# Performance work log

Hardware: AMD Instinct MI355X
Metric: run time of the kernel (lower is better)

Reference implementation:

```python
import jax, jax.numpy as jnp
import numpy as np

MAX_DISP = 4                    # R: max displacement of the correlation window
D = 2 * MAX_DISP + 1            # window side -> D*D = 81 offset channels


def setup_inputs() -> dict:
    key = jax.random.key(0)
    k1, k2 = jax.random.split(key)
    B, C, H, W = 16, 256, 96, 96
    reference_features = jax.random.normal(k1, (B, D * D, H, W), dtype=jnp.float32)
    query_features = jax.random.normal(k2, (B, C, H, W), dtype=jnp.float32)
    return {"reference_features": reference_features, "query_features": query_features}


def reference(reference_features, query_features):
    # reference_features: [B, D*D, H, W] correlation volume (weights per spatial offset)
    # query_features:     [B, C, H, W]  feature map
    # out[b,c,y,x] = sum_{dy,dx in [-R,R]} corr[b, idx(dy,dx), y-dy, x-dx] * feat[b,c,y-dy,x-dx]
    # i.e. the adjoint of local correlation: scatter-accumulate across shifted windows.
    B, D2, H, W = reference_features.shape
    C = query_features.shape[1]
    R = MAX_DISP
    # Padded accumulator so every shifted write stays in-bounds (zero padding semantics).
    acc = jnp.zeros((B, C, H + 2 * R, W + 2 * R), dtype=query_features.dtype)
    for idx in range(D2):  # fixed small offset set (81), not a data-dim loop
        dy = idx // D - R
        dx = idx % D - R
        w = reference_features[:, idx:idx + 1] * query_features  # [B, C, H, W]
        acc = acc.at[:, :, R + dy:R + dy + H, R + dx:R + dx + W].add(w)
    return acc[:, :, R:R + H, R:R + W]
```

## Files before the change

### kernel.cpp

```cpp
#include <hip/hip_runtime.h>


#define RR 4
#define DD 9
#define D2 81
#define Bn 16
#define Cn 256
#define Hn 96
#define Wn 96
#define HWn (Hn*Wn)
#define NTH 512
#define KW  104

typedef __attribute__((ext_vector_type(8))) short bf16x8;
typedef __attribute__((ext_vector_type(4))) float f32x4;

__device__ __forceinline__ ushort f2bf(float f) {
    uint u = __float_as_uint(f);
    return (ushort)((u + 0x7FFFu + ((u >> 16) & 1u)) >> 16);
}

__global__ __launch_bounds__(NTH, 2)
void corrT11_kernel(const float* __restrict__ corr,
                    const float* __restrict__ feat,
                    float* __restrict__ out)
{
    __shared__ ushort A_sh[2][Cn][KW];
    __shared__ ushort M_sh[2][Wn][KW];

    int bid = blockIdx.x;
    int L   = (bid & 7) * 192 + (bid >> 3);
    int y   = L % Hn;
    int b   = L / Hn;

    const int tid  = threadIdx.x;
    const int lane = tid & 63;
    const int wid  = tid >> 6;
    const int mrow = lane & 15;
    const int kgrp = (lane >> 4) << 3;

    {
        uint* p = (uint*)A_sh;
        for (int t = tid; t < (int)(sizeof(A_sh) / 4); t += NTH) p[t] = 0u;
        uint* q = (uint*)M_sh;
        for (int t = tid; t < (int)(sizeof(M_sh) / 4); t += NTH) q[t] = 0u;
    }
    __syncthreads();

    const int klo = max(0, y - (Hn - 1 - RR));
    const int khi = min(DD - 1, y + RR);

    const int ac  = tid >> 1;
    const int seg = tid & 1;
    const float* fbase = feat + (((size_t)b * Cn + ac) * Hn) * Wn + seg * 48;

    {
        const int sy = y + RR - klo;
        const float* src = fbase + (size_t)sy * Wn;
        #pragma unroll
        for (int i = 0; i < 12; ++i) {
            float4 v = *reinterpret_cast<const float4*>(src + i * 4);
            uint lo = (uint)f2bf(v.x) | ((uint)f2bf(v.y) << 16);
            uint hi = (uint)f2bf(v.z) | ((uint)f2bf(v.w) << 16);
            *reinterpret_cast<uint2*>(&A_sh[0][ac][4 + seg * 48 + i * 4]) = make_uint2(lo, hi);
        }
        for (int t = tid; t < DD * Wn; t += NTH) {
            int kdx = t / Wn;
            int x   = t - kdx * Wn;
            int sx  = x + RR - kdx;
            int sxc = min(max(sx, 0), Wn - 1);
            float v = corr[((size_t)b * D2 + klo * DD + kdx) * HWn + sy * Wn + sxc];
            M_sh[0][x][x + 2 * RR - kdx] = f2bf(v);
        }
    }

    f32x4 acc[2][6];
    #pragma unroll
    for (int ct = 0; ct < 2; ++ct)
        #pragma unroll
        for (int xt = 0; xt < 6; ++xt)
            acc[ct][xt] = (f32x4){0.f, 0.f, 0.f, 0.f};

    #pragma unroll 1
    for (int kk = klo; kk <= khi; ++kk) {
        const int pb = (kk - klo) & 1;
        __syncthreads();

        const bool vn = (kk + 1 <= khi);
        float4 fv[12];
        float  mv0 = 0.f, mv1 = 0.f;
        if (vn) {
            const int sy = y + RR - (kk + 1);
            const float* src = fbase + (size_t)sy * Wn;
            #pragma unroll
            for (int i = 0; i < 12; ++i)
                fv[i] = *reinterpret_cast<const float4*>(src + i * 4);
            {
                int t = tid;
                int kdx = t / Wn, x = t - kdx * Wn;
                int sx  = x + RR - kdx;
                int sxc = min(max(sx, 0), Wn - 1);
                mv0 = corr[((size_t)b * D2 + (kk + 1) * DD + kdx) * HWn + sy * Wn + sxc];
            }
            if (tid + NTH < DD * Wn) {
                int t = tid + NTH;
                int kdx = t / Wn, x = t - kdx * Wn;
                int sx  = x + RR - kdx;
                int sxc = min(max(sx, 0), Wn - 1);
                mv1 = corr[((size_t)b * D2 + (kk + 1) * DD + kdx) * HWn + sy * Wn + sxc];
            }
        }

        #pragma unroll
        for (int xt = 0; xt < 6; ++xt) {
            const int kb = (xt == 5) ? 72 : xt * 16;
            bf16x8 bfr = *reinterpret_cast<const bf16x8*>(&M_sh[pb][xt * 16 + mrow][kb + kgrp]);
            #pragma unroll
            for (int ct = 0; ct < 2; ++ct) {
                bf16x8 afr = *reinterpret_cast<const bf16x8*>(&A_sh[pb][wid * 32 + ct * 16 + mrow][kb + kgrp]);
                acc[ct][xt] = __builtin_amdgcn_mfma_f32_16x16x32_bf16(afr, bfr, acc[ct][xt], 0, 0, 0);
            }
        }

        if (vn) {
            #pragma unroll
            for (int i = 0; i < 12; ++i) {
                uint lo = (uint)f2bf(fv[i].x) | ((uint)f2bf(fv[i].y) << 16);
                uint hi = (uint)f2bf(fv[i].z) | ((uint)f2bf(fv[i].w) << 16);
                *reinterpret_cast<uint2*>(&A_sh[pb ^ 1][ac][4 + seg * 48 + i * 4]) = make_uint2(lo, hi);
            }
            {
                int t = tid;
                int kdx = t / Wn, x = t - kdx * Wn;
                M_sh[pb ^ 1][x][x + 2 * RR - kdx] = f2bf(mv0);
            }
            if (tid + NTH < DD * Wn) {
                int t = tid + NTH;
                int kdx = t / Wn, x = t - kdx * Wn;
                M_sh[pb ^ 1][x][x + 2 * RR - kdx] = f2bf(mv1);
            }
        }
    }

    const int csub = (lane >> 4) << 2;
    #pragma unroll
    for (int ct = 0; ct < 2; ++ct) {
        #pragma unroll
        for (int xt = 0; xt < 6; ++xt) {
            #pragma unroll
            for (int r = 0; r < 4; ++r) {
                int c = wid * 32 + ct * 16 + csub + r;
                int x = xt * 16 + mrow;
                out[(((size_t)b * Cn + c) * Hn + y) * Wn + x] = acc[ct][xt][r];
            }
        }
    }
}

extern "C" void kernel_launch(void* const* d_in, const int* in_sizes, int n_in,
                              void* d_out, int out_size, void* d_ws, size_t ws_size,
                              hipStream_t stream)
{
    const float* corr = (const float*)d_in[0];
    const float* feat = (const float*)d_in[1];
    float* out = (float*)d_out;

    const int grid = Bn * Hn;
    corrT11_kernel<<<grid, NTH, 0, stream>>>(corr, feat, out);
}
```

Before: 190.5 us.

## Shrink LDS footprint with compact M tiles and single-buffered A to raise occupancy

```diff
diff --git a/kernel.cpp b/kernel.cpp
--- a/kernel.cpp
+++ b/kernel.cpp
@@ -11,22 +11,28 @@
 #define HWn (Hn*Wn)
 #define NTH 512
 #define KW  104
+#define MW  36
 
 typedef __attribute__((ext_vector_type(8))) short bf16x8;
 typedef __attribute__((ext_vector_type(4))) float f32x4;
 
+__device__ __forceinline__ uint cvt_pk(float lo, float hi) {
+    uint r;
+    asm("v_cvt_pk_bf16_f32 %0, %1, %2" : "=v"(r) : "v"(lo), "v"(hi));
+    return r;
+}
 __device__ __forceinline__ ushort f2bf(float f) {
     uint u = __float_as_uint(f);
     return (ushort)((u + 0x7FFFu + ((u >> 16) & 1u)) >> 16);
 }
 
-__global__ __launch_bounds__(NTH, 2)
-void corrT11_kernel(const float* __restrict__ corr,
+__global__ __launch_bounds__(NTH, 4)
+void corrT13_kernel(const float* __restrict__ corr,
                     const float* __restrict__ feat,
                     float* __restrict__ out)
 {
-    __shared__ ushort A_sh[2][Cn][KW];
-    __shared__ ushort M_sh[2][Wn][KW];
+    __shared__ ushort A_sh[Cn][KW];
+    __shared__ ushort M_sh[2][Wn][MW];
 
     int bid = blockIdx.x;
     int L   = (bid & 7) * 192 + (bid >> 3);
@@ -37,14 +43,14 @@
     const int lane = tid & 63;
     const int wid  = tid >> 6;
     const int mrow = lane & 15;
-    const int kgrp = (lane >> 4) << 3;
+    const int kq   = lane >> 4;
+    const int kgrp = kq << 3;
 
-    {
-        uint* p = (uint*)A_sh;
-        for (int t = tid; t < (int)(sizeof(A_sh) / 4); t += NTH) p[t] = 0u;
-        uint* q = (uint*)M_sh;
-        for (int t = tid; t < (int)(sizeof(M_sh) / 4); t += NTH) q[t] = 0u;
+    for (int i = tid; i < Cn; i += NTH) {
+        *reinterpret_cast<uint2*>(&A_sh[i][0])   = make_uint2(0u, 0u);
+        *reinterpret_cast<uint2*>(&A_sh[i][100]) = make_uint2(0u, 0u);
     }
+    for (int i = tid; i < (int)(sizeof(M_sh) / 4); i += NTH) ((uint*)M_sh)[i] = 0u;
     __syncthreads();
 
     const int klo = max(0, y - (Hn - 1 - RR));
@@ -60,101 +66,108 @@
         #pragma unroll
         for (int i = 0; i < 12; ++i) {
             float4 v = *reinterpret_cast<const float4*>(src + i * 4);
-            uint lo = (uint)f2bf(v.x) | ((uint)f2bf(v.y) << 16);
-            uint hi = (uint)f2bf(v.z) | ((uint)f2bf(v.w) << 16);
-            *reinterpret_cast<uint2*>(&A_sh[0][ac][4 + seg * 48 + i * 4]) = make_uint2(lo, hi);
+            *reinterpret_cast<uint2*>(&A_sh[ac][4 + seg * 48 + i * 4])
+                = make_uint2(cvt_pk(v.x, v.y), cvt_pk(v.z, v.w));
         }
         for (int t = tid; t < DD * Wn; t += NTH) {
-            int kdx = t / Wn;
-            int x   = t - kdx * Wn;
-            int sx  = x + RR - kdx;
-            int sxc = min(max(sx, 0), Wn - 1);
-            float v = corr[((size_t)b * D2 + klo * DD + kdx) * HWn + sy * Wn + sxc];
-            M_sh[0][x][x + 2 * RR - kdx] = f2bf(v);
+            int kdx = t / Wn, x = t - kdx * Wn;
+            int sxp = x + 2 * RR - kdx;
+            int kbx = (x >= 80) ? 72 : (x & ~15);
+            int sxc = min(max(sxp - RR, 0), Wn - 1);
+            M_sh[0][x][sxp - kbx] = f2bf(corr[((size_t)b * D2 + klo * DD + kdx) * HWn + sy * Wn + sxc]);
         }
     }
+    __syncthreads();
 
     f32x4 acc[2][6];
     #pragma unroll
     for (int ct = 0; ct < 2; ++ct)
         #pragma unroll
-        for (int xt = 0; xt < 6; ++xt)
-            acc[ct][xt] = (f32x4){0.f, 0.f, 0.f, 0.f};
+        for (int t6 = 0; t6 < 6; ++t6)
+            acc[ct][t6] = (f32x4){0.f, 0.f, 0.f, 0.f};
 
     #pragma unroll 1
     for (int kk = klo; kk <= khi; ++kk) {
         const int pb = (kk - klo) & 1;
-        __syncthreads();
+        const bool vn = (kk + 1 <= khi);
+        const float* srcn = fbase + (size_t)(y + RR - (kk + 1)) * Wn;
 
-        const bool vn = (kk + 1 <= khi);
-        float4 fv[12];
-        float  mv0 = 0.f, mv1 = 0.f;
+        float4 fv0, fv1, fv2, fv3, fv4, fv5;
+        float mv0 = 0.f, mv1 = 0.f;
         if (vn) {
-            const int sy = y + RR - (kk + 1);
-            const float* src = fbase + (size_t)sy * Wn;
-            #pragma unroll
-            for (int i = 0; i < 12; ++i)
-                fv[i] = *reinterpret_cast<const float4*>(src + i * 4);
+            fv0 = *reinterpret_cast<const float4*>(srcn);
+            fv1 = *reinterpret_cast<const float4*>(srcn + 4);
+            fv2 = *reinterpret_cast<const float4*>(srcn + 8);
+            fv3 = *reinterpret_cast<const float4*>(srcn + 12);
+            fv4 = *reinterpret_cast<const float4*>(srcn + 16);
+            fv5 = *reinterpret_cast<const float4*>(srcn + 20);
+            const int syn = y + RR - (kk + 1);
             {
-                int t = tid;
-                int kdx = t / Wn, x = t - kdx * Wn;
-                int sx  = x + RR - kdx;
-                int sxc = min(max(sx, 0), Wn - 1);
-                mv0 = corr[((size_t)b * D2 + (kk + 1) * DD + kdx) * HWn + sy * Wn + sxc];
+                int t = tid, kdx = t / Wn, x = t - kdx * Wn;
+                int sxc = min(max(x + RR - kdx, 0), Wn - 1);
+                mv0 = corr[((size_t)b * D2 + (kk + 1) * DD + kdx) * HWn + syn * Wn + sxc];
             }
             if (tid + NTH < DD * Wn) {
-                int t = tid + NTH;
-                int kdx = t / Wn, x = t - kdx * Wn;
-                int sx  = x + RR - kdx;
-                int sxc = min(max(sx, 0), Wn - 1);
-                mv1 = corr[((size_t)b * D2 + (kk + 1) * DD + kdx) * HWn + sy * Wn + sxc];
+                int t = tid + NTH, kdx = t / Wn, x = t - kdx * Wn;
+                int sxc = min(max(x + RR - kdx, 0), Wn - 1);
+                mv1 = corr[((size_t)b * D2 + (kk + 1) * DD + kdx) * HWn + syn * Wn + sxc];
             }
         }
 
         #pragma unroll
-        for (int xt = 0; xt < 6; ++xt) {
-            const int kb = (xt == 5) ? 72 : xt * 16;
-            bf16x8 bfr = *reinterpret_cast<const bf16x8*>(&M_sh[pb][xt * 16 + mrow][kb + kgrp]);
+        for (int t6 = 0; t6 < 6; ++t6) {
+            const int kb = (t6 == 5) ? 72 : t6 * 16;
+            const ushort* mp = &M_sh[pb][t6 * 16 + mrow][kgrp];
+            uint2 m0 = *reinterpret_cast<const uint2*>(mp);
+            uint2 m1 = *reinterpret_cast<const uint2*>(mp + 4);
+            uint4 bw = make_uint4(m0.x, m0.y, m1.x, m1.y);
+            bf16x8 bfr = *reinterpret_cast<bf16x8*>(&bw);
             #pragma unroll
             for (int ct = 0; ct < 2; ++ct) {
-                bf16x8 afr = *reinterpret_cast<const bf16x8*>(&A_sh[pb][wid * 32 + ct * 16 + mrow][kb + kgrp]);
-                acc[ct][xt] = __builtin_amdgcn_mfma_f32_16x16x32_bf16(afr, bfr, acc[ct][xt], 0, 0, 0);
+                bf16x8 afr = *reinterpret_cast<const bf16x8*>(&A_sh[wid * 32 + ct * 16 + mrow][kb + kgrp]);
+                acc[ct][t6] = __builtin_amdgcn_mfma_f32_16x16x32_bf16(afr, bfr, acc[ct][t6], 0, 0, 0);
             }
         }
+        __syncthreads();
 
         if (vn) {
+            *reinterpret_cast<uint2*>(&A_sh[ac][4 + seg * 48 + 0])  = make_uint2(cvt_pk(fv0.x, fv0.y), cvt_pk(fv0.z, fv0.w));
+            *reinterpret_cast<uint2*>(&A_sh[ac][4 + seg * 48 + 4])  = make_uint2(cvt_pk(fv1.x, fv1.y), cvt_pk(fv1.z, fv1.w));
+            *reinterpret_cast<uint2*>(&A_sh[ac][4 + seg * 48 + 8])  = make_uint2(cvt_pk(fv2.x, fv2.y), cvt_pk(fv2.z, fv2.w));
+            *reinterpret_cast<uint2*>(&A_sh[ac][4 + seg * 48 + 12]) = make_uint2(cvt_pk(fv3.x, fv3.y), cvt_pk(fv3.z, fv3.w));
+            *reinterpret_cast<uint2*>(&A_sh[ac][4 + seg * 48 + 16]) = make_uint2(cvt_pk(fv4.x, fv4.y), cvt_pk(fv4.z, fv4.w));
+            *reinterpret_cast<uint2*>(&A_sh[ac][4 + seg * 48 + 20]) = make_uint2(cvt_pk(fv5.x, fv5.y), cvt_pk(fv5.z, fv5.w));
             #pragma unroll
-            for (int i = 0; i < 12; ++i) {
-                uint lo = (uint)f2bf(fv[i].x) | ((uint)f2bf(fv[i].y) << 16);
-                uint hi = (uint)f2bf(fv[i].z) | ((uint)f2bf(fv[i].w) << 16);
-                *reinterpret_cast<uint2*>(&A_sh[pb ^ 1][ac][4 + seg * 48 + i * 4]) = make_uint2(lo, hi);
+            for (int i = 6; i < 12; ++i) {
+                float4 v = *reinterpret_cast<const float4*>(srcn + i * 4);
+                *reinterpret_cast<uint2*>(&A_sh[ac][4 + seg * 48 + i * 4])
+                    = make_uint2(cvt_pk(v.x, v.y), cvt_pk(v.z, v.w));
             }
             {
-                int t = tid;
-                int kdx = t / Wn, x = t - kdx * Wn;
-                M_sh[pb ^ 1][x][x + 2 * RR - kdx] = f2bf(mv0);
+                int t = tid, kdx = t / Wn, x = t - kdx * Wn;
+                int sxp = x + 2 * RR - kdx;
+                int kbx = (x >= 80) ? 72 : (x & ~15);
+                M_sh[pb ^ 1][x][sxp - kbx] = f2bf(mv0);
             }
             if (tid + NTH < DD * Wn) {
-                int t = tid + NTH;
-                int kdx = t / Wn, x = t - kdx * Wn;
-                M_sh[pb ^ 1][x][x + 2 * RR - kdx] = f2bf(mv1);
+                int t = tid + NTH, kdx = t / Wn, x = t - kdx * Wn;
+                int sxp = x + 2 * RR - kdx;
+                int kbx = (x >= 80) ? 72 : (x & ~15);
+                M_sh[pb ^ 1][x][sxp - kbx] = f2bf(mv1);
             }
         }
+        __syncthreads();
     }
 
-    const int csub = (lane >> 4) << 2;
+    const int csub = kq << 2;
     #pragma unroll
-    for (int ct = 0; ct < 2; ++ct) {
+    for (int ct = 0; ct < 2; ++ct)
         #pragma unroll
-        for (int xt = 0; xt < 6; ++xt) {
+        for (int t6 = 0; t6 < 6; ++t6)
             #pragma unroll
-            for (int r = 0; r < 4; ++r) {
-                int c = wid * 32 + ct * 16 + csub + r;
-                int x = xt * 16 + mrow;
-                out[(((size_t)b * Cn + c) * Hn + y) * Wn + x] = acc[ct][xt][r];
-            }
-        }
-    }
+            for (int r = 0; r < 4; ++r)
+                out[(((size_t)b * Cn + wid * 32 + ct * 16 + csub + r) * Hn + y) * Wn + t6 * 16 + mrow]
+                    = acc[ct][t6][r];
 }
 
 extern "C" void kernel_launch(void* const* d_in, const int* in_sizes, int n_in,
@@ -166,5 +179,5 @@
     float* out = (float*)d_out;
 
     const int grid = Bn * Hn;
-    corrT11_kernel<<<grid, NTH, 0, stream>>>(corr, feat, out);
+    corrT13_kernel<<<grid, NTH, 0, stream>>>(corr, feat, out);
 }
```

Result: slower. 316.9 us (+66.3%).
